# Performance work log

Measured on AMD Instinct MI355X. Metric: run time of the kernel, lower is better.

The kernel has to match this reference:

```python
import jax, jax.numpy as jnp
import numpy as np

DATA_DIM = 4096
BATCH = 16384


def _make_perm(data_dim: int, seed: int = 0) -> np.ndarray:
    # Mirrors PermutationalLayer.__init__: pair even/odd indices, permute the
    # pairs (guaranteed non-identity), then flatten back to a D-length perm.
    rng = np.random.default_rng(seed)
    data_idx = np.stack([np.arange(0, data_dim, 2), np.arange(1, data_dim, 2)], axis=0)  # [2, D/2]
    n = data_dim // 2
    perm = rng.permutation(n)
    while np.array_equal(perm, np.arange(n)):
        perm = rng.permutation(n)
    return data_idx[:, perm].T.flatten().astype(np.int64)  # [D]


def setup_inputs() -> dict:
    key = jax.random.key(0)
    z = jax.random.normal(key, (BATCH, DATA_DIM), dtype=jnp.float32)
    perm_idx = jnp.asarray(_make_perm(DATA_DIM))
    return {"z": z, "perm_idx": perm_idx}


def reference(z, perm_idx):
    # Original: z @ perm.T with perm = eye(D)[perm_idx].
    # (z @ perm.T)[b, i] = z[b, perm_idx[i]]  ->  a pure gather along the last dim.
    return jnp.take(z, perm_idx, axis=-1)
```

## Files before the change

### kernel.cpp

```cpp
#include <hip/hip_runtime.h>


#define DATA_DIM 4096
#define PAIRS    (DATA_DIM / 2)
#define QUADS    (DATA_DIM / 4)
#define BLOCK    256

__global__ __launch_bounds__(BLOCK) void perm_gather_kernel(
    const float2* __restrict__ z2,
    const int4*   __restrict__ pidx4,
    float4*       __restrict__ out4)
{
    const int row = blockIdx.x;
    const float2* __restrict__ zrow = z2 + (size_t)row * PAIRS;
    float4* __restrict__ orow       = out4 + (size_t)row * QUADS;

    const int t = threadIdx.x;
#pragma unroll
    for (int q = t; q < QUADS; q += BLOCK) {
        const int4 p = pidx4[q];
        const float2 a = zrow[p.x >> 1];
        const float2 b = zrow[p.z >> 1];
        orow[q] = make_float4(a.x, a.y, b.x, b.y);
    }
}

extern "C" void kernel_launch(void* const* d_in, const int* in_sizes, int n_in,
                              void* d_out, int out_size, void* d_ws, size_t ws_size,
                              hipStream_t stream) {
    const float2* z2    = (const float2*)d_in[0];
    const int4*   pidx4 = (const int4*)d_in[1];
    float4*       out4  = (float4*)d_out;

    const int batch = in_sizes[0] / DATA_DIM;

    perm_gather_kernel<<<batch, BLOCK, 0, stream>>>(z2, pidx4, out4);
}
```

Before: 492.9 us.

## Stage rows in LDS with coalesced loads and gather from shared memory

Each block now loads two full rows of z into shared memory using coalesced float4 loads, synchronises, and then performs the permutation gather from LDS. Each index load is reused across both rows. This replaces scattered 8-byte global reads with contiguous 16-byte reads. In exchange it uses 32KB of LDS per block, which can reduce occupancy, and adds a barrier that serialises the load and gather phases within a block.

```diff
diff --git a/kernel.cpp b/kernel.cpp
--- a/kernel.cpp
+++ b/kernel.cpp
@@ -5,34 +5,49 @@
 #define PAIRS    (DATA_DIM / 2)
 #define QUADS    (DATA_DIM / 4)
 #define BLOCK    256
+#define ROWS     2
 
-__global__ __launch_bounds__(BLOCK) void perm_gather_kernel(
-    const float2* __restrict__ z2,
+__global__ __launch_bounds__(BLOCK) void perm_gather_lds_kernel(
+    const float4* __restrict__ z4,
     const int4*   __restrict__ pidx4,
     float4*       __restrict__ out4)
 {
-    const int row = blockIdx.x;
-    const float2* __restrict__ zrow = z2 + (size_t)row * PAIRS;
-    float4* __restrict__ orow       = out4 + (size_t)row * QUADS;
+    __shared__ float2 srow[ROWS][PAIRS];
 
-    const int t = threadIdx.x;
+    const int row0 = blockIdx.x * ROWS;
+    const int t    = threadIdx.x;
+
+#pragma unroll
+    for (int r = 0; r < ROWS; ++r) {
+        const float4* __restrict__ zrow = z4 + (size_t)(row0 + r) * QUADS;
+        float4* s4 = (float4*)srow[r];
+#pragma unroll
+        for (int q = t; q < QUADS; q += BLOCK)
+            s4[q] = zrow[q];
+    }
+    __syncthreads();
+
 #pragma unroll
     for (int q = t; q < QUADS; q += BLOCK) {
-        const int4 p = pidx4[q];
-        const float2 a = zrow[p.x >> 1];
-        const float2 b = zrow[p.z >> 1];
-        orow[q] = make_float4(a.x, a.y, b.x, b.y);
+        const int4 p  = pidx4[q];
+        const int  ia = p.x >> 1;
+        const int  ib = p.z >> 1;
+#pragma unroll
+        for (int r = 0; r < ROWS; ++r) {
+            const float2 a = srow[r][ia];
+            const float2 b = srow[r][ib];
+            out4[(size_t)(row0 + r) * QUADS + q] = make_float4(a.x, a.y, b.x, b.y);
+        }
     }
 }
 
 extern "C" void kernel_launch(void* const* d_in, const int* in_sizes, int n_in,
                               void* d_out, int out_size, void* d_ws, size_t ws_size,
                               hipStream_t stream) {
-    const float2* z2    = (const float2*)d_in[0];
+    const float4* z4    = (const float4*)d_in[0];
     const int4*   pidx4 = (const int4*)d_in[1];
     float4*       out4  = (float4*)d_out;
 
     const int batch = in_sizes[0] / DATA_DIM;
-
-    perm_gather_kernel<<<batch, BLOCK, 0, stream>>>(z2, pidx4, out4);
+    perm_gather_lds_kernel<<<batch / ROWS, BLOCK, 0, stream>>>(z4, pidx4, out4);
 }
```

After: 431.3 us. 1.14x faster.

## Stage each row in LDS via global_load_lds, then gather from shared memory

Applied to the files above, without the earlier changes.

Each block now copies its whole 16 KB input row into LDS with coalesced 16-byte direct global-to-LDS loads. It then does the pair permutation as LDS reads instead of scattered 8-byte global gathers. Index loads are hoisted into registers ahead of the copy. This replaces uncoalesced global reads with fully coalesced streaming. The cost is 16 KB of LDS per block and a barrier, and the code depends on the gfx950 16-byte global_load_lds builtin and on how its per-lane LDS pointer is handled.

```diff
diff --git a/kernel.cpp b/kernel.cpp
--- a/kernel.cpp
+++ b/kernel.cpp
@@ -5,34 +5,50 @@
 #define PAIRS    (DATA_DIM / 2)
 #define QUADS    (DATA_DIM / 4)
 #define BLOCK    256
+#define PER_T    (QUADS / BLOCK)
 
-__global__ __launch_bounds__(BLOCK) void perm_gather_kernel(
-    const float2* __restrict__ z2,
+__global__ __launch_bounds__(BLOCK) void perm_gather_lds_kernel(
+    const float4* __restrict__ z4,
     const int4*   __restrict__ pidx4,
     float4*       __restrict__ out4)
 {
+    __shared__ float4 s4[QUADS];
+
     const int row = blockIdx.x;
-    const float2* __restrict__ zrow = z2 + (size_t)row * PAIRS;
-    float4* __restrict__ orow       = out4 + (size_t)row * QUADS;
+    const int t   = threadIdx.x;
+    const float4* __restrict__ zrow = z4 + (size_t)row * QUADS;
 
-    const int t = threadIdx.x;
+    int4 p[PER_T];
 #pragma unroll
-    for (int q = t; q < QUADS; q += BLOCK) {
-        const int4 p = pidx4[q];
-        const float2 a = zrow[p.x >> 1];
-        const float2 b = zrow[p.z >> 1];
-        orow[q] = make_float4(a.x, a.y, b.x, b.y);
+    for (int k = 0; k < PER_T; ++k)
+        p[k] = pidx4[t + k * BLOCK];
+
+#pragma unroll
+    for (int k = 0; k < PER_T; ++k) {
+        __builtin_amdgcn_global_load_lds(
+            (const __attribute__((address_space(1))) void*)(zrow + t + k * BLOCK),
+            (__attribute__((address_space(3))) void*)(s4 + t + k * BLOCK),
+            16, 0, 0);
+    }
+    __syncthreads();
+
+    const float2* s2 = (const float2*)s4;
+    float4* __restrict__ orow = out4 + (size_t)row * QUADS;
+#pragma unroll
+    for (int k = 0; k < PER_T; ++k) {
+        const float2 a = s2[p[k].x >> 1];
+        const float2 b = s2[p[k].z >> 1];
+        orow[t + k * BLOCK] = make_float4(a.x, a.y, b.x, b.y);
     }
 }
 
 extern "C" void kernel_launch(void* const* d_in, const int* in_sizes, int n_in,
                               void* d_out, int out_size, void* d_ws, size_t ws_size,
                               hipStream_t stream) {
-    const float2* z2    = (const float2*)d_in[0];
+    const float4* z4    = (const float4*)d_in[0];
     const int4*   pidx4 = (const int4*)d_in[1];
     float4*       out4  = (float4*)d_out;
 
     const int batch = in_sizes[0] / DATA_DIM;
-
-    perm_gather_kernel<<<batch, BLOCK, 0, stream>>>(z2, pidx4, out4);
+    perm_gather_lds_kernel<<<batch, BLOCK, 0, stream>>>(z4, pidx4, out4);
 }
```

Measured after the change: 421.3 us. 14.5% less time.
